# Kernel optimization log

Hardware: AMD Instinct MI355X
Metric: run time of the kernel (lower is better)

The kernel has to match this reference:

```python
import jax, jax.numpy as jnp
import numpy as np

B, C, T, H, W = 1024, 1, 500, 7, 7
HID, OUT = 16, 2


def setup_inputs() -> dict:
    key = jax.random.key(0)
    k1, k2, k3, k4 = jax.random.split(key, 4)
    rppg_embeddings = jax.random.normal(k1, (B, C, T, H, W), dtype=jnp.float32)
    rBr = jax.random.normal(k2, (B, C, T), dtype=jnp.float32)
    # final_dense_layer params: Linear(500,16) -> Dropout (identity at eval) -> Linear(16,2)
    W1 = jax.random.normal(k3, (C * T, HID), dtype=jnp.float32) / np.sqrt(C * T)
    b1 = jnp.zeros((HID,), dtype=jnp.float32)
    W2 = jax.random.normal(k4, (HID, OUT), dtype=jnp.float32) / np.sqrt(HID)
    b2 = jnp.zeros((OUT,), dtype=jnp.float32)
    return {"rppg_embeddings": rppg_embeddings, "rBr": rBr,
            "W1": W1, "b1": b1, "W2": W2, "b2": b2}


def reference(rppg_embeddings, rBr, W1, b1, W2, b2):
    # AvgPool3d(kernel=[1,7,7], stride=1, pad=0) on (B,C,T,7,7) -> (B,C,T,1,1):
    # equivalent to mean over the full 7x7 spatial window.
    x = jnp.mean(rppg_embeddings, axis=(-2, -1))            # (B, C, T)
    # batched FFT phase along time (replaces the per-(b,c) Python loop)
    phase = jnp.angle(jnp.fft.fft(x, axis=-1))              # (B, C, T)
    flat = phase.reshape(phase.shape[0], -1)                # (B, C*T) = (B, 500)
    h = flat @ W1 + b1                                      # (B, 16); dropout = identity (eval)
    rBP = h @ W2 + b2                                       # (B, 2)
    return rBP
```

## Files before the change

### kernel.cpp

```cpp
#include <hip/hip_runtime.h>
#include <math.h>

#ifndef M_PI
#define M_PI 3.14159265358979323846
#endif

#define T_LEN 500
#define HW49  49
#define HID   16
#define NOUT  2

__global__ __launch_bounds__(256, 4) void bp_fused2_kernel(
    const float* __restrict__ rppg,
    const float* __restrict__ W1,
    const float* __restrict__ b1,
    const float* __restrict__ W2,
    const float* __restrict__ b2,
    float* __restrict__ out)
{
    __shared__ __align__(16) float stage[2][3136];
    __shared__ __align__(16) float xsh[512];
    __shared__ float wsum[4][HID + 1];
    const int tid = threadIdx.x;
    const int row = blockIdx.x;
    const float4* src4 = (const float4*)(rppg + (size_t)row * (T_LEN * HW49));

    if (tid < 12) xsh[T_LEN + tid] = 0.f;

    const float4 fz = {0.f, 0.f, 0.f, 0.f};
    float4 r0, r1, r2, r3;

    r0 = src4[tid]; r1 = src4[tid + 256]; r2 = src4[tid + 512];
    r3 = (tid < 16) ? src4[tid + 768] : fz;
    {
        float4* st = (float4*)stage[0];
        st[tid] = r0; st[tid + 256] = r1; st[tid + 512] = r2;
        if (tid < 16) st[tid + 768] = r3;
    }
    __syncthreads();

    const int bin  = tid >> 2;
    const int part = tid & 3;
    const int nels = (part < 3) ? 13 : 10;
    const int boff = bin * HW49 + part * 13;

    for (int c = 0; c < 8; ++c) {
        if (c < 7) {
            const int n4 = (c + 1 < 7) ? 784 : 637;
            const float4* b4 = src4 + 784 * (c + 1);
            r0 = (tid       < n4) ? b4[tid      ] : fz;
            r1 = (tid + 256 < n4) ? b4[tid + 256] : fz;
            r2 = (tid + 512 < n4) ? b4[tid + 512] : fz;
            r3 = (tid + 768 < n4) ? b4[tid + 768] : fz;
        }
        const int bins_c = (c < 7) ? 64 : 52;
        {
            const float* bufp = stage[c & 1];
            float s = 0.f;
            if (bin < bins_c) {
                const float* p = bufp + boff;
                for (int j = 0; j < nels; ++j) s += p[j];
            }
            s += __shfl_xor(s, 1);
            s += __shfl_xor(s, 2);
            if (part == 0 && bin < bins_c) xsh[c * 64 + bin] = s * (1.0f / 49.0f);
        }
        __syncthreads();
        if (c < 7) {
            const int n4 = (c + 1 < 7) ? 784 : 637;
            float4* st = (float4*)stage[(c + 1) & 1];
            if (tid       < n4) st[tid      ] = r0;
            if (tid + 256 < n4) st[tid + 256] = r1;
            if (tid + 512 < n4) st[tid + 512] = r2;
            if (tid + 768 < n4) st[tid + 768] = r3;
            __syncthreads();
        }
    }

    float hp[HID];
    #pragma unroll
    for (int j = 0; j < HID; ++j) hp[j] = 0.f;

    if (tid <= 249) {
        const int k = tid;
        const double ang = (double)k * (-2.0 * M_PI / 500.0);
        double c1, s1;
        sincos(ang, &s1, &c1);
        const double c2 = fma(c1, c1, -(s1 * s1));
        const double s2 = 2.0 * c1 * s1;
        const float c1f = (float)c1, s1f = (float)s1;
        const float c2f = (float)c2, s2f = (float)s2;
        const float c3f = (float)fma(c1, c2, -(s1 * s2));
        const float s3f = (float)fma(c1, s2,  (s1 * c2));
        const float c4f = (float)fma(c2, c2, -(s2 * s2));
        const float s4f = (float)(2.0 * c2 * s2);

        float cw = 1.f, sw = 0.f;
        float re0 = 0.f, im0 = 0.f, re1 = 0.f, im1 = 0.f;
        float re2 = 0.f, im2 = 0.f, re3 = 0.f, im3 = 0.f;
        const float4* x4 = (const float4*)xsh;
        float4 xv = x4[0];
        for (int j = 0; j < 125; ++j) {
            const float4 nx = x4[j + 1];
            re0 = fmaf(xv.x, cw, re0); im0 = fmaf(xv.x, sw, im0);
            re1 = fmaf(xv.y, cw, re1); im1 = fmaf(xv.y, sw, im1);
            re2 = fmaf(xv.z, cw, re2); im2 = fmaf(xv.z, sw, im2);
            re3 = fmaf(xv.w, cw, re3); im3 = fmaf(xv.w, sw, im3);
            const float tc = fmaf(cw, c4f, -(sw * s4f));
            sw = fmaf(cw, s4f, sw * c4f);
            cw = tc;
            xv = nx;
        }
        const float re = re0 + fmaf(c1f, re1, -(s1f * im1))
                             + fmaf(c2f, re2, -(s2f * im2))
                             + fmaf(c3f, re3, -(s3f * im3));
        const float im = im0 + fmaf(c1f, im1,  (s1f * re1))
                             + fmaf(c2f, im2,  (s2f * re2))
                             + fmaf(c3f, im3,  (s3f * re3));
        const float ph = atan2f(im, re);

        if (k == 0) {
            const float* w = W1;
            #pragma unroll
            for (int j = 0; j < HID; ++j) hp[j] = ph * w[j];
        } else {
            const float* wa = W1 + k * HID;
            const float* wb = W1 + (T_LEN - k) * HID;
            #pragma unroll
            for (int j = 0; j < HID; ++j) hp[j] = ph * (wa[j] - wb[j]);
        }
    }

    #pragma unroll
    for (int j = 0; j < HID; ++j) {
        float v = hp[j];
        v += __shfl_xor(v, 1);  v += __shfl_xor(v, 2);
        v += __shfl_xor(v, 4);  v += __shfl_xor(v, 8);
        v += __shfl_xor(v, 16); v += __shfl_xor(v, 32);
        hp[j] = v;
    }
    if ((tid & 63) == 0) {
        const int w = tid >> 6;
        #pragma unroll
        for (int j = 0; j < HID; ++j) wsum[w][j] = hp[j];
    }
    __syncthreads();

    if (tid < NOUT) {
        const int o = tid;
        float acc = b2[o];
        #pragma unroll
        for (int j = 0; j < HID; ++j) {
            const float h = wsum[0][j] + wsum[1][j] + wsum[2][j] + wsum[3][j] + b1[j];
            acc = fmaf(h, W2[j * NOUT + o], acc);
        }
        out[row * NOUT + o] = acc;
    }
}

extern "C" void kernel_launch(void* const* d_in, const int* in_sizes, int n_in,
                              void* d_out, int out_size, void* d_ws, size_t ws_size,
                              hipStream_t stream) {
    const float* rppg = (const float*)d_in[0];
    const float* W1 = (const float*)d_in[2];
    const float* b1 = (const float*)d_in[3];
    const float* W2 = (const float*)d_in[4];
    const float* b2 = (const float*)d_in[5];
    float* out = (float*)d_out;

    bp_fused2_kernel<<<dim3(1024), dim3(256), 0, stream>>>(rppg, W1, b1, W2, b2, out);
}
```

Measured before the change: 167.5 us.

## Split fused pooling+DFT kernel into separate pool and DFT-head kernels

```diff
diff --git a/kernel.cpp b/kernel.cpp
--- a/kernel.cpp
+++ b/kernel.cpp
@@ -10,72 +10,51 @@
 #define HID   16
 #define NOUT  2
 
-__global__ __launch_bounds__(256, 4) void bp_fused2_kernel(
-    const float* __restrict__ rppg,
+__global__ __launch_bounds__(256) void pool_kernel(
+    const float* __restrict__ rppg, float* __restrict__ xout)
+{
+    const int n   = blockIdx.x * 256 + threadIdx.x;
+    const int row = n / 125;
+    const int g   = n - row * 125;
+    const float4* g4 = (const float4*)rppg + (size_t)row * 6125 + g * 49;
+
+    float acc[4] = {0.f, 0.f, 0.f, 0.f};
+    #pragma unroll
+    for (int j = 0; j < 49; ++j) {
+        const float4 v = g4[j];
+        acc[(4 * j + 0) / 49] += v.x;
+        acc[(4 * j + 1) / 49] += v.y;
+        acc[(4 * j + 2) / 49] += v.z;
+        acc[(4 * j + 3) / 49] += v.w;
+    }
+    float4 o;
+    o.x = acc[0] * (1.0f / 49.0f);
+    o.y = acc[1] * (1.0f / 49.0f);
+    o.z = acc[2] * (1.0f / 49.0f);
+    o.w = acc[3] * (1.0f / 49.0f);
+    *(float4*)(xout + (size_t)row * T_LEN + g * 4) = o;
+}
+
+__global__ __launch_bounds__(256, 4) void dft_head_kernel(
+    const float* __restrict__ xin,
     const float* __restrict__ W1,
     const float* __restrict__ b1,
     const float* __restrict__ W2,
     const float* __restrict__ b2,
     float* __restrict__ out)
 {
-    __shared__ __align__(16) float stage[2][3136];
     __shared__ __align__(16) float xsh[512];
     __shared__ float wsum[4][HID + 1];
     const int tid = threadIdx.x;
     const int row = blockIdx.x;
-    const float4* src4 = (const float4*)(rppg + (size_t)row * (T_LEN * HW49));
-
-    if (tid < 12) xsh[T_LEN + tid] = 0.f;
-
-    const float4 fz = {0.f, 0.f, 0.f, 0.f};
-    float4 r0, r1, r2, r3;
-
-    r0 = src4[tid]; r1 = src4[tid + 256]; r2 = src4[tid + 512];
-    r3 = (tid < 16) ? src4[tid + 768] : fz;
+
     {
-        float4* st = (float4*)stage[0];
-        st[tid] = r0; st[tid + 256] = r1; st[tid + 512] = r2;
-        if (tid < 16) st[tid + 768] = r3;
-    }
-    __syncthreads();
-
-    const int bin  = tid >> 2;
-    const int part = tid & 3;
-    const int nels = (part < 3) ? 13 : 10;
-    const int boff = bin * HW49 + part * 13;
-
-    for (int c = 0; c < 8; ++c) {
-        if (c < 7) {
-            const int n4 = (c + 1 < 7) ? 784 : 637;
-            const float4* b4 = src4 + 784 * (c + 1);
-            r0 = (tid       < n4) ? b4[tid      ] : fz;
-            r1 = (tid + 256 < n4) ? b4[tid + 256] : fz;
-            r2 = (tid + 512 < n4) ? b4[tid + 512] : fz;
-            r3 = (tid + 768 < n4) ? b4[tid + 768] : fz;
-        }
-        const int bins_c = (c < 7) ? 64 : 52;
-        {
-            const float* bufp = stage[c & 1];
-            float s = 0.f;
-            if (bin < bins_c) {
-                const float* p = bufp + boff;
-                for (int j = 0; j < nels; ++j) s += p[j];
-            }
-            s += __shfl_xor(s, 1);
-            s += __shfl_xor(s, 2);
-            if (part == 0 && bin < bins_c) xsh[c * 64 + bin] = s * (1.0f / 49.0f);
-        }
-        __syncthreads();
-        if (c < 7) {
-            const int n4 = (c + 1 < 7) ? 784 : 637;
-            float4* st = (float4*)stage[(c + 1) & 1];
-            if (tid       < n4) st[tid      ] = r0;
-            if (tid + 256 < n4) st[tid + 256] = r1;
-            if (tid + 512 < n4) st[tid + 512] = r2;
-            if (tid + 768 < n4) st[tid + 768] = r3;
-            __syncthreads();
-        }
-    }
+        float4* x4s = (float4*)xsh;
+        const float4* xr4 = (const float4*)(xin + (size_t)row * T_LEN);
+        if (tid < 125) x4s[tid] = xr4[tid];
+        else if (tid < 128) x4s[tid] = float4{0.f, 0.f, 0.f, 0.f};
+    }
+    __syncthreads();
 
     float hp[HID];
     #pragma unroll
@@ -158,6 +137,143 @@
     }
 }
 
+__global__ __launch_bounds__(256, 4) void bp_fused2_kernel(
+    const float* __restrict__ rppg,
+    const float* __restrict__ W1, const float* __restrict__ b1,
+    const float* __restrict__ W2, const float* __restrict__ b2,
+    float* __restrict__ out)
+{
+    __shared__ __align__(16) float stage[2][3136];
+    __shared__ __align__(16) float xsh[512];
+    __shared__ float wsum[4][HID + 1];
+    const int tid = threadIdx.x;
+    const int row = blockIdx.x;
+    const float4* src4 = (const float4*)(rppg + (size_t)row * (T_LEN * HW49));
+
+    if (tid < 12) xsh[T_LEN + tid] = 0.f;
+    const float4 fz = {0.f, 0.f, 0.f, 0.f};
+    float4 r0, r1, r2, r3;
+    r0 = src4[tid]; r1 = src4[tid + 256]; r2 = src4[tid + 512];
+    r3 = (tid < 16) ? src4[tid + 768] : fz;
+    {
+        float4* st = (float4*)stage[0];
+        st[tid] = r0; st[tid + 256] = r1; st[tid + 512] = r2;
+        if (tid < 16) st[tid + 768] = r3;
+    }
+    __syncthreads();
+    const int bin  = tid >> 2;
+    const int part = tid & 3;
+    const int nels = (part < 3) ? 13 : 10;
+    const int boff = bin * HW49 + part * 13;
+    for (int c = 0; c < 8; ++c) {
+        if (c < 7) {
+            const int n4 = (c + 1 < 7) ? 784 : 637;
+            const float4* b4 = src4 + 784 * (c + 1);
+            r0 = (tid       < n4) ? b4[tid      ] : fz;
+            r1 = (tid + 256 < n4) ? b4[tid + 256] : fz;
+            r2 = (tid + 512 < n4) ? b4[tid + 512] : fz;
+            r3 = (tid + 768 < n4) ? b4[tid + 768] : fz;
+        }
+        const int bins_c = (c < 7) ? 64 : 52;
+        {
+            const float* bufp = stage[c & 1];
+            float s = 0.f;
+            if (bin < bins_c) {
+                const float* p = bufp + boff;
+                for (int j = 0; j < nels; ++j) s += p[j];
+            }
+            s += __shfl_xor(s, 1);
+            s += __shfl_xor(s, 2);
+            if (part == 0 && bin < bins_c) xsh[c * 64 + bin] = s * (1.0f / 49.0f);
+        }
+        __syncthreads();
+        if (c < 7) {
+            const int n4 = (c + 1 < 7) ? 784 : 637;
+            float4* st = (float4*)stage[(c + 1) & 1];
+            if (tid       < n4) st[tid      ] = r0;
+            if (tid + 256 < n4) st[tid + 256] = r1;
+            if (tid + 512 < n4) st[tid + 512] = r2;
+            if (tid + 768 < n4) st[tid + 768] = r3;
+            __syncthreads();
+        }
+    }
+
+    float hp[HID];
+    #pragma unroll
+    for (int j = 0; j < HID; ++j) hp[j] = 0.f;
+    if (tid <= 249) {
+        const int k = tid;
+        const double ang = (double)k * (-2.0 * M_PI / 500.0);
+        double c1, s1;
+        sincos(ang, &s1, &c1);
+        const double c2 = fma(c1, c1, -(s1 * s1));
+        const double s2 = 2.0 * c1 * s1;
+        const float c1f = (float)c1, s1f = (float)s1;
+        const float c2f = (float)c2, s2f = (float)s2;
+        const float c3f = (float)fma(c1, c2, -(s1 * s2));
+        const float s3f = (float)fma(c1, s2,  (s1 * c2));
+        const float c4f = (float)fma(c2, c2, -(s2 * s2));
+        const float s4f = (float)(2.0 * c2 * s2);
+        float cw = 1.f, sw = 0.f;
+        float re0 = 0.f, im0 = 0.f, re1 = 0.f, im1 = 0.f;
+        float re2 = 0.f, im2 = 0.f, re3 = 0.f, im3 = 0.f;
+        const float4* x4 = (const float4*)xsh;
+        float4 xv = x4[0];
+        for (int j = 0; j < 125; ++j) {
+            const float4 nx = x4[j + 1];
+            re0 = fmaf(xv.x, cw, re0); im0 = fmaf(xv.x, sw, im0);
+            re1 = fmaf(xv.y, cw, re1); im1 = fmaf(xv.y, sw, im1);
+            re2 = fmaf(xv.z, cw, re2); im2 = fmaf(xv.z, sw, im2);
+            re3 = fmaf(xv.w, cw, re3); im3 = fmaf(xv.w, sw, im3);
+            const float tc = fmaf(cw, c4f, -(sw * s4f));
+            sw = fmaf(cw, s4f, sw * c4f);
+            cw = tc;
+            xv = nx;
+        }
+        const float re = re0 + fmaf(c1f, re1, -(s1f * im1))
+                             + fmaf(c2f, re2, -(s2f * im2))
+                             + fmaf(c3f, re3, -(s3f * im3));
+        const float im = im0 + fmaf(c1f, im1,  (s1f * re1))
+                             + fmaf(c2f, im2,  (s2f * re2))
+                             + fmaf(c3f, im3,  (s3f * re3));
+        const float ph = atan2f(im, re);
+        if (k == 0) {
+            const float* w = W1;
+            #pragma unroll
+            for (int j = 0; j < HID; ++j) hp[j] = ph * w[j];
+        } else {
+            const float* wa = W1 + k * HID;
+            const float* wb = W1 + (T_LEN - k) * HID;
+            #pragma unroll
+            for (int j = 0; j < HID; ++j) hp[j] = ph * (wa[j] - wb[j]);
+        }
+    }
+    #pragma unroll
+    for (int j = 0; j < HID; ++j) {
+        float v = hp[j];
+        v += __shfl_xor(v, 1);  v += __shfl_xor(v, 2);
+        v += __shfl_xor(v, 4);  v += __shfl_xor(v, 8);
+        v += __shfl_xor(v, 16); v += __shfl_xor(v, 32);
+        hp[j] = v;
+    }
+    if ((tid & 63) == 0) {
+        const int w = tid >> 6;
+        #pragma unroll
+        for (int j = 0; j < HID; ++j) wsum[w][j] = hp[j];
+    }
+    __syncthreads();
+    if (tid < NOUT) {
+        const int o = tid;
+        float acc = b2[o];
+        #pragma unroll
+        for (int j = 0; j < HID; ++j) {
+            const float h = wsum[0][j] + wsum[1][j] + wsum[2][j] + wsum[3][j] + b1[j];
+            acc = fmaf(h, W2[j * NOUT + o], acc);
+        }
+        out[row * NOUT + o] = acc;
+    }
+}
+
 extern "C" void kernel_launch(void* const* d_in, const int* in_sizes, int n_in,
                               void* d_out, int out_size, void* d_ws, size_t ws_size,
                               hipStream_t stream) {
@@ -168,5 +284,12 @@
     const float* b2 = (const float*)d_in[5];
     float* out = (float*)d_out;
 
-    bp_fused2_kernel<<<dim3(1024), dim3(256), 0, stream>>>(rppg, W1, b1, W2, b2, out);
-}
+    const size_t need = (size_t)1024 * T_LEN * sizeof(float);
+    if (ws_size >= need) {
+        float* x = (float*)d_ws;
+        pool_kernel<<<dim3(500), dim3(256), 0, stream>>>(rppg, x);
+        dft_head_kernel<<<dim3(1024), dim3(256), 0, stream>>>(x, W1, b1, W2, b2, out);
+    } else {
+        bp_fused2_kernel<<<dim3(1024), dim3(256), 0, stream>>>(rppg, W1, b1, W2, b2, out);
+    }
+}
```

New measurement: 186.9 us. 11.6% more time.

## Stage input in four larger chunks with deeper register prefetch

Applied to the files above, without the earlier changes.

```diff
diff --git a/kernel.cpp b/kernel.cpp
--- a/kernel.cpp
+++ b/kernel.cpp
@@ -10,7 +10,7 @@
 #define HID   16
 #define NOUT  2
 
-__global__ __launch_bounds__(256, 4) void bp_fused2_kernel(
+__global__ __launch_bounds__(256) void bp_fused3_kernel(
     const float* __restrict__ rppg,
     const float* __restrict__ W1,
     const float* __restrict__ b1,
@@ -18,7 +18,8 @@
     const float* __restrict__ b2,
     float* __restrict__ out)
 {
-    __shared__ __align__(16) float stage[2][3136];
+    __shared__ __align__(16) float buf0[6272];
+    __shared__ __align__(16) float buf1[6272];
     __shared__ __align__(16) float xsh[512];
     __shared__ float wsum[4][HID + 1];
     const int tid = threadIdx.x;
@@ -27,55 +28,105 @@
 
     if (tid < 12) xsh[T_LEN + tid] = 0.f;
 
-    const float4 fz = {0.f, 0.f, 0.f, 0.f};
-    float4 r0, r1, r2, r3;
-
-    r0 = src4[tid]; r1 = src4[tid + 256]; r2 = src4[tid + 512];
-    r3 = (tid < 16) ? src4[tid + 768] : fz;
-    {
-        float4* st = (float4*)stage[0];
-        st[tid] = r0; st[tid + 256] = r1; st[tid + 512] = r2;
-        if (tid < 16) st[tid + 768] = r3;
-    }
-    __syncthreads();
-
-    const int bin  = tid >> 2;
-    const int part = tid & 3;
-    const int nels = (part < 3) ? 13 : 10;
-    const int boff = bin * HW49 + part * 13;
-
-    for (int c = 0; c < 8; ++c) {
-        if (c < 7) {
-            const int n4 = (c + 1 < 7) ? 784 : 637;
-            const float4* b4 = src4 + 784 * (c + 1);
-            r0 = (tid       < n4) ? b4[tid      ] : fz;
-            r1 = (tid + 256 < n4) ? b4[tid + 256] : fz;
-            r2 = (tid + 512 < n4) ? b4[tid + 512] : fz;
-            r3 = (tid + 768 < n4) ? b4[tid + 768] : fz;
-        }
-        const int bins_c = (c < 7) ? 64 : 52;
-        {
-            const float* bufp = stage[c & 1];
-            float s = 0.f;
-            if (bin < bins_c) {
-                const float* p = bufp + boff;
-                for (int j = 0; j < nels; ++j) s += p[j];
-            }
-            s += __shfl_xor(s, 1);
-            s += __shfl_xor(s, 2);
-            if (part == 0 && bin < bins_c) xsh[c * 64 + bin] = s * (1.0f / 49.0f);
-        }
-        __syncthreads();
-        if (c < 7) {
-            const int n4 = (c + 1 < 7) ? 784 : 637;
-            float4* st = (float4*)stage[(c + 1) & 1];
-            if (tid       < n4) st[tid      ] = r0;
-            if (tid + 256 < n4) st[tid + 256] = r1;
-            if (tid + 512 < n4) st[tid + 512] = r2;
-            if (tid + 768 < n4) st[tid + 768] = r3;
-            __syncthreads();
-        }
-    }
+    const int bin  = tid >> 1;
+    const int part = tid & 1;
+    const int nsum = part ? 24 : 25;
+    const int soff = part * 25;
+
+    float4 r[7];
+
+    #pragma unroll
+    for (int s = 0; s < 7; ++s) {
+        const int i = tid + 256 * s;
+        if (i < 1568) r[s] = src4[i];
+    }
+    {
+        float4 q[6];
+        #pragma unroll
+        for (int s = 0; s < 6; ++s) {
+            const int i = tid + 256 * s;
+            if (i < 1519) q[s] = src4[1568 + i];
+        }
+        float4* d0 = (float4*)buf0;
+        #pragma unroll
+        for (int s = 0; s < 7; ++s) {
+            const int i = tid + 256 * s;
+            if (i < 1568) d0[i] = r[s];
+        }
+        float4* d1 = (float4*)buf1;
+        #pragma unroll
+        for (int s = 0; s < 6; ++s) {
+            const int i = tid + 256 * s;
+            if (i < 1519) d1[i] = q[s];
+        }
+    }
+    __syncthreads();
+
+    {
+        float s = 0.f;
+        const float* p = buf0 + bin * HW49 + soff;
+        #pragma unroll
+        for (int j = 0; j < 25; ++j) if (j < nsum) s += p[j];
+        s += __shfl_xor(s, 1);
+        if (!part) xsh[bin] = s * (1.0f / 49.0f);
+    }
+    __syncthreads();
+
+    #pragma unroll
+    for (int s = 0; s < 6; ++s) {
+        const int i = tid + 256 * s;
+        if (i < 1519) r[s] = src4[3087 + i];
+    }
+    {
+        float4* d0 = (float4*)buf0;
+        #pragma unroll
+        for (int s = 0; s < 6; ++s) {
+            const int i = tid + 256 * s;
+            if (i < 1519) d0[i] = r[s];
+        }
+    }
+    if (bin < 124) {
+        float s = 0.f;
+        const float* p = buf1 + bin * HW49 + soff;
+        #pragma unroll
+        for (int j = 0; j < 25; ++j) if (j < nsum) s += p[j];
+        s += __shfl_xor(s, 1);
+        if (!part) xsh[128 + bin] = s * (1.0f / 49.0f);
+    }
+    __syncthreads();
+
+    #pragma unroll
+    for (int s = 0; s < 6; ++s) {
+        const int i = tid + 256 * s;
+        if (i < 1519) r[s] = src4[4606 + i];
+    }
+    {
+        float4* d1 = (float4*)buf1;
+        #pragma unroll
+        for (int s = 0; s < 6; ++s) {
+            const int i = tid + 256 * s;
+            if (i < 1519) d1[i] = r[s];
+        }
+    }
+    if (bin < 124) {
+        float s = 0.f;
+        const float* p = buf0 + bin * HW49 + soff;
+        #pragma unroll
+        for (int j = 0; j < 25; ++j) if (j < nsum) s += p[j];
+        s += __shfl_xor(s, 1);
+        if (!part) xsh[252 + bin] = s * (1.0f / 49.0f);
+    }
+    __syncthreads();
+
+    if (bin < 124) {
+        float s = 0.f;
+        const float* p = buf1 + bin * HW49 + soff;
+        #pragma unroll
+        for (int j = 0; j < 25; ++j) if (j < nsum) s += p[j];
+        s += __shfl_xor(s, 1);
+        if (!part) xsh[376 + bin] = s * (1.0f / 49.0f);
+    }
+    __syncthreads();
 
     float hp[HID];
     #pragma unroll
@@ -168,5 +219,5 @@
     const float* b2 = (const float*)d_in[5];
     float* out = (float*)d_out;
 
-    bp_fused2_kernel<<<dim3(1024), dim3(256), 0, stream>>>(rppg, W1, b1, W2, b2, out);
+    bp_fused3_kernel<<<dim3(1024), dim3(256), 0, stream>>>(rppg, W1, b1, W2, b2, out);
 }
```

After: 204.5 us. 22.1% more time.

## Load spatial slabs directly into LDS per wave with global_load_lds

Applied to the files above, without the earlier changes.

```diff
diff --git a/kernel.cpp b/kernel.cpp
--- a/kernel.cpp
+++ b/kernel.cpp
@@ -10,7 +10,7 @@
 #define HID   16
 #define NOUT  2
 
-__global__ __launch_bounds__(256, 4) void bp_fused2_kernel(
+__global__ __launch_bounds__(256) void bp_fused4_kernel(
     const float* __restrict__ rppg,
     const float* __restrict__ W1,
     const float* __restrict__ b1,
@@ -18,64 +18,75 @@
     const float* __restrict__ b2,
     float* __restrict__ out)
 {
-    __shared__ __align__(16) float stage[2][3136];
+    __shared__ __align__(16) float slab[12544];
     __shared__ __align__(16) float xsh[512];
     __shared__ float wsum[4][HID + 1];
-    const int tid = threadIdx.x;
-    const int row = blockIdx.x;
+    const int tid  = threadIdx.x;
+    const int wave = tid >> 6;
+    const int lane = tid & 63;
+    const int row  = blockIdx.x;
     const float4* src4 = (const float4*)(rppg + (size_t)row * (T_LEN * HW49));
 
     if (tid < 12) xsh[T_LEN + tid] = 0.f;
 
-    const float4 fz = {0.f, 0.f, 0.f, 0.f};
-    float4 r0, r1, r2, r3;
+    float4* const lseg = ((float4*)slab) + wave * 784;
+    const float* const lsegf = (const float*)lseg;
 
-    r0 = src4[tid]; r1 = src4[tid + 256]; r2 = src4[tid + 512];
-    r3 = (tid < 16) ? src4[tid + 768] : fz;
     {
-        float4* st = (float4*)stage[0];
-        st[tid] = r0; st[tid + 256] = r1; st[tid + 512] = r2;
-        if (tid < 16) st[tid + 768] = r3;
+        const int f4off = wave * 784;
+        const int nf4   = (wave < 3) ? 784 : 735;
+        const int bin0  = wave * 64;
+        const int nbin  = (wave < 3) ? 64 : 60;
+        const float4* g4 = src4 + f4off;
+        #pragma unroll
+        for (int call = 0; call < 13; ++call) {
+            const int idx = call * 64 + lane;
+            if (idx < nf4) {
+                __builtin_amdgcn_global_load_lds(
+                    (const __attribute__((address_space(1))) void*)(g4 + idx),
+                    (__attribute__((address_space(3))) void*)(lseg + call * 64),
+                    16, 0, 0);
+            }
+        }
+        __builtin_amdgcn_s_waitcnt(0);
+        __builtin_amdgcn_sched_barrier(0);
+        if (lane < nbin) {
+            const float* p = lsegf + lane * HW49;
+            float s = 0.f;
+            #pragma unroll
+            for (int j = 0; j < HW49; ++j) s += p[j];
+            xsh[bin0 + lane] = s * (1.0f / 49.0f);
+        }
+        __builtin_amdgcn_sched_barrier(0);
+    }
+
+    {
+        const int f4off = 3087 + wave * 784;
+        const int nf4   = (wave < 3) ? 784 : 686;
+        const int bin0  = 252 + wave * 64;
+        const int nbin  = (wave < 3) ? 64 : 56;
+        const float4* g4 = src4 + f4off;
+        #pragma unroll
+        for (int call = 0; call < 13; ++call) {
+            const int idx = call * 64 + lane;
+            if (idx < nf4) {
+                __builtin_amdgcn_global_load_lds(
+                    (const __attribute__((address_space(1))) void*)(g4 + idx),
+                    (__attribute__((address_space(3))) void*)(lseg + call * 64),
+                    16, 0, 0);
+            }
+        }
+        __builtin_amdgcn_s_waitcnt(0);
+        __builtin_amdgcn_sched_barrier(0);
+        if (lane < nbin) {
+            const float* p = lsegf + lane * HW49;
+            float s = 0.f;
+            #pragma unroll
+            for (int j = 0; j < HW49; ++j) s += p[j];
+            xsh[bin0 + lane] = s * (1.0f / 49.0f);
+        }
     }
     __syncthreads();
-
-    const int bin  = tid >> 2;
-    const int part = tid & 3;
-    const int nels = (part < 3) ? 13 : 10;
-    const int boff = bin * HW49 + part * 13;
-
-    for (int c = 0; c < 8; ++c) {
-        if (c < 7) {
-            const int n4 = (c + 1 < 7) ? 784 : 637;
-            const float4* b4 = src4 + 784 * (c + 1);
-            r0 = (tid       < n4) ? b4[tid      ] : fz;
-            r1 = (tid + 256 < n4) ? b4[tid + 256] : fz;
-            r2 = (tid + 512 < n4) ? b4[tid + 512] : fz;
-            r3 = (tid + 768 < n4) ? b4[tid + 768] : fz;
-        }
-        const int bins_c = (c < 7) ? 64 : 52;
-        {
-            const float* bufp = stage[c & 1];
-            float s = 0.f;
-            if (bin < bins_c) {
-                const float* p = bufp + boff;
-                for (int j = 0; j < nels; ++j) s += p[j];
-            }
-            s += __shfl_xor(s, 1);
-            s += __shfl_xor(s, 2);
-            if (part == 0 && bin < bins_c) xsh[c * 64 + bin] = s * (1.0f / 49.0f);
-        }
-        __syncthreads();
-        if (c < 7) {
-            const int n4 = (c + 1 < 7) ? 784 : 637;
-            float4* st = (float4*)stage[(c + 1) & 1];
-            if (tid       < n4) st[tid      ] = r0;
-            if (tid + 256 < n4) st[tid + 256] = r1;
-            if (tid + 512 < n4) st[tid + 512] = r2;
-            if (tid + 768 < n4) st[tid + 768] = r3;
-            __syncthreads();
-        }
-    }
 
     float hp[HID];
     #pragma unroll
@@ -139,10 +150,9 @@
         v += __shfl_xor(v, 16); v += __shfl_xor(v, 32);
         hp[j] = v;
     }
-    if ((tid & 63) == 0) {
-        const int w = tid >> 6;
+    if (lane == 0) {
         #pragma unroll
-        for (int j = 0; j < HID; ++j) wsum[w][j] = hp[j];
+        for (int j = 0; j < HID; ++j) wsum[wave][j] = hp[j];
     }
     __syncthreads();
 
@@ -168,5 +178,5 @@
     const float* b2 = (const float*)d_in[5];
     float* out = (float*)d_out;
 
-    bp_fused2_kernel<<<dim3(1024), dim3(256), 0, stream>>>(rppg, W1, b1, W2, b2, out);
+    bp_fused4_kernel<<<dim3(1024), dim3(256), 0, stream>>>(rppg, W1, b1, W2, b2, out);
 }
```

Result: faster. 157.8 us (-5.8%).
